# Optimization experiments

Measured on AMD Instinct MI355X. Metric: run time of the kernel, lower is better.

Reference implementation:

```python
import jax, jax.numpy as jnp
import numpy as np

DIM = 512
HEADS = 8
WIN = 64
HIDDEN = 2048
EPS = 1e-5


def layernorm(x, g, b):
    mu = jnp.mean(x, axis=-1, keepdims=True)
    var = jnp.var(x, axis=-1, keepdims=True)
    return (x - mu) * jax.lax.rsqrt(var + EPS) * g + b


def setup_inputs() -> dict:
    key = jax.random.key(0)
    ks = jax.random.split(key, 10)
    s = lambda fan_in: 1.0 / np.sqrt(fan_in)
    return {
        "x": jax.random.normal(ks[0], (8, 4096, DIM), dtype=jnp.float32),
        "ln1_g": jnp.ones((DIM,), jnp.float32),
        "ln1_b": jnp.zeros((DIM,), jnp.float32),
        "qkv_w": jax.random.normal(ks[1], (DIM, 3 * DIM), jnp.float32) * s(DIM),
        "qkv_b": jnp.zeros((3 * DIM,), jnp.float32),
        "proj_w": jax.random.normal(ks[2], (DIM, DIM), jnp.float32) * s(DIM),
        "proj_b": jnp.zeros((DIM,), jnp.float32),
        "ln2_g": jnp.ones((DIM,), jnp.float32),
        "ln2_b": jnp.zeros((DIM,), jnp.float32),
        "fc1_w": jax.random.normal(ks[3], (DIM, HIDDEN), jnp.float32) * s(DIM),
        "fc1_b": jnp.zeros((HIDDEN,), jnp.float32),
        "fc2_w": jax.random.normal(ks[4], (HIDDEN, DIM), jnp.float32) * s(HIDDEN),
        "fc2_b": jnp.zeros((DIM,), jnp.float32),
    }


def reference(x, ln1_g, ln1_b, qkv_w, qkv_b, proj_w, proj_b, ln2_g, ln2_b,
              fc1_w, fc1_b, fc2_w, fc2_b):
    B, N, C = x.shape
    hd = C // HEADS
    scale = hd ** -0.5

    # --- W-MSA (shift_size forced to 0, attn_mask None) ---
    h = layernorm(x, ln1_g, ln1_b)
    hw = h.reshape(B * (N // WIN), WIN, C)
    qkv = hw @ qkv_w + qkv_b
    qkv = qkv.reshape(-1, WIN, 3, HEADS, hd)
    q = qkv[:, :, 0] * scale
    k = qkv[:, :, 1]
    v = qkv[:, :, 2]
    attn = jnp.einsum('bqhd,bkhd->bhqk', q, k)
    attn = jax.nn.softmax(attn, axis=-1)
    o = jnp.einsum('bhqk,bkhd->bqhd', attn, v).reshape(-1, WIN, C)
    o = o @ proj_w + proj_b
    x = x + o.reshape(B, N, C)

    # --- MLP (GELU exact, dropout=0) ---
    h2 = layernorm(x, ln2_g, ln2_b)
    h2 = jax.nn.gelu(h2 @ fc1_w + fc1_b, approximate=False)
    x = x + (h2 @ fc2_w + fc2_b)
    return x
```

## Files before the change

### kernel.cpp

```cpp
#include <hip/hip_runtime.h>
#include <hip/hip_bf16.h>
#include <cstdint>

typedef unsigned short U16;
typedef float f32x4 __attribute__((ext_vector_type(4)));
typedef __bf16 bf16x8 __attribute__((ext_vector_type(8)));

#define DEVINL __device__ __forceinline__

DEVINL U16 f2bf(float f) {
    unsigned u = __float_as_uint(f);
    return (U16)((u + 0x7FFFu + ((u >> 16) & 1u)) >> 16);
}
DEVINL float bf2f(U16 s) { return __uint_as_float(((unsigned)s) << 16); }

DEVINL void gld16(const void* g, void* l) {
    __builtin_amdgcn_global_load_lds(
        (const __attribute__((address_space(1))) void*)g,
        (__attribute__((address_space(3))) void*)l, 16, 0, 0);
}

#define MFMA_BF16 __builtin_amdgcn_mfma_f32_16x16x32_bf16

__global__ __launch_bounds__(256) void tcast_kernel(const float* __restrict__ w,
                                                    U16* __restrict__ wt, int K, int N) {
    __shared__ float tile[32][33];
    int n0 = blockIdx.x * 32, k0 = blockIdx.y * 32;
    int tx = threadIdx.x, ty = threadIdx.y;
#pragma unroll
    for (int i = 0; i < 32; i += 8) tile[ty + i][tx] = w[(size_t)(k0 + ty + i) * N + (n0 + tx)];
    __syncthreads();
#pragma unroll
    for (int i = 0; i < 32; i += 8) wt[(size_t)(n0 + ty + i) * K + (k0 + tx)] = f2bf(tile[tx][ty + i]);
}

__global__ __launch_bounds__(256) void ln_kernel(const float* __restrict__ x,
                                                 const float* __restrict__ g,
                                                 const float* __restrict__ b,
                                                 U16* __restrict__ out) {
    int lane = threadIdx.x & 63;
    size_t row = (size_t)blockIdx.x * 4 + (threadIdx.x >> 6);
    const float4* xr = (const float4*)(x + row * 512);
    float4 v0 = xr[lane], v1 = xr[lane + 64];
    float s = (v0.x + v0.y) + (v0.z + v0.w) + (v1.x + v1.y) + (v1.z + v1.w);
    float sq = (v0.x * v0.x + v0.y * v0.y + v0.z * v0.z + v0.w * v0.w) +
               (v1.x * v1.x + v1.y * v1.y + v1.z * v1.z + v1.w * v1.w);
#pragma unroll
    for (int m = 1; m < 64; m <<= 1) { s += __shfl_xor(s, m); sq += __shfl_xor(sq, m); }
    float mu = s * (1.f / 512.f);
    float var = sq * (1.f / 512.f) - mu * mu;
    float rs = rsqrtf(var + 1e-5f);
    const float4* g4 = (const float4*)g;
    const float4* b4 = (const float4*)b;
    float4 gv = g4[lane], bv = b4[lane];
    ushort4 o;
    o.x = f2bf((v0.x - mu) * rs * gv.x + bv.x);
    o.y = f2bf((v0.y - mu) * rs * gv.y + bv.y);
    o.z = f2bf((v0.z - mu) * rs * gv.z + bv.z);
    o.w = f2bf((v0.w - mu) * rs * gv.w + bv.w);
    ((ushort4*)(out + row * 512))[lane] = o;
    gv = g4[lane + 64]; bv = b4[lane + 64];
    o.x = f2bf((v1.x - mu) * rs * gv.x + bv.x);
    o.y = f2bf((v1.y - mu) * rs * gv.y + bv.y);
    o.z = f2bf((v1.z - mu) * rs * gv.z + bv.z);
    o.w = f2bf((v1.w - mu) * rs * gv.w + bv.w);
    ((ushort4*)(out + row * 512))[lane + 64] = o;
}

template <int EPI>
__global__ __launch_bounds__(512, 1) void gemm256(const U16* __restrict__ A,
                                                  const U16* __restrict__ Bt,
                                                  const float* __restrict__ bias,
                                                  const float* __restrict__ resid,
                                                  U16* __restrict__ outb,
                                                  float* __restrict__ outf,
                                                  int M, int N, int K, int gridN) {
    __shared__ __align__(16) U16 smem[65536];

    const int tid = threadIdx.x;
    const int lane = tid & 63, wv = tid >> 6;
    const int lo = lane & 15, hi = lane >> 4;
    const int wm = wv >> 2, wn = wv & 3;

    const int nwg = gridDim.x, bid = blockIdx.x;
    const int swz = (bid & 7) * (nwg >> 3) + (bid >> 3);
    const int bn = swz % gridN, bm = swz / gridN;

    const int sr = tid >> 3;
    const int clog = (tid & 7) ^ (sr & 7);
    const U16* gA = A + (size_t)(bm * 256 + sr) * K + clog * 8;
    const U16* gB = Bt + (size_t)(bn * 256 + sr) * K + clog * 8;

#define STAGE_PANEL(g, off, p)                                        \
    do {                                                              \
        U16* _l = smem + (off) + (p) * 8192 + tid * 8;                \
        gld16((g) + (size_t)((p) * 128) * K, _l);                     \
        gld16((g) + (size_t)((p) * 128 + 64) * K, _l + 4096);         \
    } while (0)

    const int ck0 = ((hi) ^ (lo & 7)) << 3;
    const int ck1 = ((4 | hi) ^ (lo & 7)) << 3;

    f32x4 acc[8][4] = {};

    STAGE_PANEL(gA, 0, 0);
    STAGE_PANEL(gB, 16384, 0);
    STAGE_PANEL(gA, 0, 1);
    STAGE_PANEL(gB, 16384, 1);
    gA += 64; gB += 64;

    const int nt = K >> 6;
    for (int t = 0; t < nt; ++t) {
        const int cb = (t & 1) << 15;
        const int nb = cb ^ 32768;
        const bool pf = (t < nt - 1);

        if (pf) {
            STAGE_PANEL(gA, nb, 0);
            asm volatile("s_waitcnt vmcnt(2)" ::: "memory");
        } else {
            asm volatile("s_waitcnt vmcnt(0)" ::: "memory");
        }
        asm volatile("s_barrier" ::: "memory");

        const U16* Ab = smem + cb + (wm * 128 + lo) * 64;
        const U16* Bb = smem + cb + 16384 + (wn * 64 + lo) * 64;

        bf16x8 af[4][2], bg[4][2];
#pragma unroll
        for (int i = 0; i < 4; ++i) {
            af[i][0] = *(const bf16x8*)(Ab + i * 1024 + ck0);
            af[i][1] = *(const bf16x8*)(Ab + i * 1024 + ck1);
        }
#pragma unroll
        for (int j = 0; j < 2; ++j) {
            bg[j][0] = *(const bf16x8*)(Bb + j * 1024 + ck0);
            bg[j][1] = *(const bf16x8*)(Bb + j * 1024 + ck1);
        }
        __builtin_amdgcn_s_setprio(1);
#pragma unroll
        for (int i = 0; i < 4; ++i)
#pragma unroll
            for (int j = 0; j < 2; ++j) {
                acc[i][j] = MFMA_BF16(af[i][0], bg[j][0], acc[i][j], 0, 0, 0);
                acc[i][j] = MFMA_BF16(af[i][1], bg[j][1], acc[i][j], 0, 0, 0);
            }
        __builtin_amdgcn_s_setprio(0);

        if (pf) STAGE_PANEL(gB, nb + 16384, 0);
#pragma unroll
        for (int j = 2; j < 4; ++j) {
            bg[j][0] = *(const bf16x8*)(Bb + j * 1024 + ck0);
            bg[j][1] = *(const bf16x8*)(Bb + j * 1024 + ck1);
        }
        __builtin_amdgcn_s_setprio(1);
#pragma unroll
        for (int i = 0; i < 4; ++i)
#pragma unroll
            for (int j = 2; j < 4; ++j) {
                acc[i][j] = MFMA_BF16(af[i][0], bg[j][0], acc[i][j], 0, 0, 0);
                acc[i][j] = MFMA_BF16(af[i][1], bg[j][1], acc[i][j], 0, 0, 0);
            }
        __builtin_amdgcn_s_setprio(0);

        if (pf) STAGE_PANEL(gA, nb, 1);
#pragma unroll
        for (int i = 0; i < 4; ++i) {
            af[i][0] = *(const bf16x8*)(Ab + (i + 4) * 1024 + ck0);
            af[i][1] = *(const bf16x8*)(Ab + (i + 4) * 1024 + ck1);
        }
        __builtin_amdgcn_s_setprio(1);
#pragma unroll
        for (int i = 0; i < 4; ++i)
#pragma unroll
            for (int j = 0; j < 2; ++j) {
                acc[4 + i][j] = MFMA_BF16(af[i][0], bg[j][0], acc[4 + i][j], 0, 0, 0);
                acc[4 + i][j] = MFMA_BF16(af[i][1], bg[j][1], acc[4 + i][j], 0, 0, 0);
            }
        __builtin_amdgcn_s_setprio(0);

        if (pf) STAGE_PANEL(gB, nb + 16384, 1);
        __builtin_amdgcn_s_setprio(1);
#pragma unroll
        for (int i = 0; i < 4; ++i)
#pragma unroll
            for (int j = 2; j < 4; ++j) {
                acc[4 + i][j] = MFMA_BF16(af[i][0], bg[j][0], acc[4 + i][j], 0, 0, 0);
                acc[4 + i][j] = MFMA_BF16(af[i][1], bg[j][1], acc[4 + i][j], 0, 0, 0);
            }
        __builtin_amdgcn_s_setprio(0);

        asm volatile("s_barrier" ::: "memory");
        gA += 64; gB += 64;
    }

    const int row0 = bm * 256 + wm * 128 + hi * 4;
    const int col0 = bn * 256 + wn * 64 + lo;
    float bc[4];
#pragma unroll
    for (int j = 0; j < 4; ++j) bc[j] = bias[col0 + j * 16];

    if (EPI == 1) {
#pragma unroll
        for (int i = 0; i < 8; ++i)
#pragma unroll
            for (int r = 0; r < 4; ++r) {
                const size_t rowb = (size_t)(row0 + i * 16 + r) * N;
#pragma unroll
                for (int j = 0; j < 4; ++j) {
                    const size_t idx = rowb + col0 + j * 16;
                    outf[idx] = acc[i][j][r] + bc[j] + resid[idx];
                }
            }
    } else {
#pragma unroll
        for (int i = 0; i < 8; ++i)
#pragma unroll
            for (int j = 0; j < 4; ++j)
#pragma unroll
                for (int r = 0; r < 4; ++r) {
                    float v = acc[i][j][r] + bc[j];
                    if (EPI == 2) v = 0.5f * v * (1.f + erff(v * 0.70710678118654752f));
                    outb[(size_t)(row0 + i * 16 + r) * N + col0 + j * 16] = f2bf(v);
                }
    }
#undef STAGE_PANEL
}

__global__ __launch_bounds__(256) void attn_kernel(const U16* __restrict__ qkv,
                                                   U16* __restrict__ o) {
    const int blk = blockIdx.x;
    const int w = blk >> 3, h = blk & 7;
    const int tid = threadIdx.x;
    const int lane = tid & 63, wv = tid >> 6;
    const int lo = lane & 15, hi = lane >> 4;

    __shared__ __align__(16) U16 Qs[64][72];
    __shared__ __align__(16) U16 Ks[64][72];
    __shared__ __align__(16) U16 Vt[64][72];
    __shared__ __align__(16) U16 Ps[4][16][72];

    {
        const int r = tid >> 2;
        const int c0 = (tid & 3) << 4;
        const U16* p = qkv + (size_t)(w * 64 + r) * 1536 + h * 64 + c0;
        *(bf16x8*)&Ks[r][c0] = *(const bf16x8*)(p + 512);
        *(bf16x8*)&Ks[r][c0 + 8] = *(const bf16x8*)(p + 520);
        const U16* pv = p + 1024;
#pragma unroll
        for (int i = 0; i < 16; i++) Vt[c0 + i][r] = pv[i];
#pragma unroll
        for (int i = 0; i < 16; i++) Qs[r][c0 + i] = f2bf(bf2f(p[i]) * 0.125f);
    }
    __syncthreads();

    const int rb = wv * 16;
    f32x4 s[4] = {};
#pragma unroll
    for (int dc = 0; dc < 64; dc += 32) {
        bf16x8 a = *(const bf16x8*)&Qs[rb + lo][dc + hi * 8];
#pragma unroll
        for (int jb = 0; jb < 4; jb++) {
            bf16x8 bfr = *(const bf16x8*)&Ks[jb * 16 + lo][dc + hi * 8];
            s[jb] = MFMA_BF16(a, bfr, s[jb], 0, 0, 0);
        }
    }
#pragma unroll
    for (int r = 0; r < 4; r++) {
        float m = fmaxf(fmaxf(s[0][r], s[1][r]), fmaxf(s[2][r], s[3][r]));
#pragma unroll
        for (int msk = 1; msk < 16; msk <<= 1) m = fmaxf(m, __shfl_xor(m, msk));
        float e[4], sum = 0.f;
#pragma unroll
        for (int jb = 0; jb < 4; jb++) { e[jb] = expf(s[jb][r] - m); sum += e[jb]; }
#pragma unroll
        for (int msk = 1; msk < 16; msk <<= 1) sum += __shfl_xor(sum, msk);
        float inv = 1.f / sum;
#pragma unroll
        for (int jb = 0; jb < 4; jb++) Ps[wv][hi * 4 + r][jb * 16 + lo] = f2bf(e[jb] * inv);
    }
    __syncthreads();

    f32x4 oa[4] = {};
#pragma unroll
    for (int jc = 0; jc < 64; jc += 32) {
        bf16x8 a = *(const bf16x8*)&Ps[wv][lo][jc + hi * 8];
#pragma unroll
        for (int db = 0; db < 4; db++) {
            bf16x8 bfr = *(const bf16x8*)&Vt[db * 16 + lo][jc + hi * 8];
            oa[db] = MFMA_BF16(a, bfr, oa[db], 0, 0, 0);
        }
    }
#pragma unroll
    for (int db = 0; db < 4; db++)
#pragma unroll
        for (int r = 0; r < 4; r++)
            o[(size_t)(w * 64 + rb + hi * 4 + r) * 512 + h * 64 + db * 16 + lo] = f2bf(oa[db][r]);
}

extern "C" void kernel_launch(void* const* d_in, const int* in_sizes, int n_in,
                              void* d_out, int out_size, void* d_ws, size_t ws_size,
                              hipStream_t stream) {
    const float* x = (const float*)d_in[0];
    const float* ln1_g = (const float*)d_in[1];
    const float* ln1_b = (const float*)d_in[2];
    const float* qkv_w = (const float*)d_in[3];
    const float* qkv_b = (const float*)d_in[4];
    const float* proj_w = (const float*)d_in[5];
    const float* proj_b = (const float*)d_in[6];
    const float* ln2_g = (const float*)d_in[7];
    const float* ln2_b = (const float*)d_in[8];
    const float* fc1_w = (const float*)d_in[9];
    const float* fc1_b = (const float*)d_in[10];
    const float* fc2_w = (const float*)d_in[11];
    const float* fc2_b = (const float*)d_in[12];
    float* out = (float*)d_out;

    char* ws = (char*)d_ws;
    U16* hbuf = (U16*)ws;
    U16* big = (U16*)(ws + 33554432);
    U16* wt_qkv = (U16*)(ws + 33554432 + 134217728);
    U16* wt_proj = wt_qkv + 1536 * 512;
    U16* wt_fc1 = wt_proj + 512 * 512;
    U16* wt_fc2 = wt_fc1 + 2048 * 512;

    dim3 tb(32, 8);
    tcast_kernel<<<dim3(1536 / 32, 512 / 32), tb, 0, stream>>>(qkv_w, wt_qkv, 512, 1536);
    tcast_kernel<<<dim3(512 / 32, 512 / 32), tb, 0, stream>>>(proj_w, wt_proj, 512, 512);
    tcast_kernel<<<dim3(2048 / 32, 512 / 32), tb, 0, stream>>>(fc1_w, wt_fc1, 512, 2048);
    tcast_kernel<<<dim3(512 / 32, 2048 / 32), tb, 0, stream>>>(fc2_w, wt_fc2, 2048, 512);

    ln_kernel<<<8192, 256, 0, stream>>>(x, ln1_g, ln1_b, hbuf);
    gemm256<0><<<768, 512, 0, stream>>>(hbuf, wt_qkv, qkv_b, nullptr, big, nullptr, 32768, 1536, 512, 6);
    attn_kernel<<<4096, 256, 0, stream>>>(big, hbuf);
    gemm256<1><<<256, 512, 0, stream>>>(hbuf, wt_proj, proj_b, x, nullptr, out, 32768, 512, 512, 2);
    ln_kernel<<<8192, 256, 0, stream>>>(out, ln2_g, ln2_b, hbuf);
    gemm256<2><<<1024, 512, 0, stream>>>(hbuf, wt_fc1, fc1_b, nullptr, big, nullptr, 32768, 2048, 512, 8);
    gemm256<1><<<256, 512, 0, stream>>>(big, wt_fc2, fc2_b, out, nullptr, out, 32768, 512, 2048, 2);
}
```

Baseline: 400.5 us.

## Restructure GEMM mainloop into 4-stage ring with 32-wide K steps

The bf16 GEMM main loop now uses 32-wide K tiles in a four-buffer LDS ring and prefetches two stages ahead. This gives one barrier per iteration and one load-then-MFMA block, replacing the interleaved double-buffered 64-wide scheme. The LDS swizzle and fragment addressing are reworked to match the 32-element rows. The launch bound now asks for two blocks per CU, which caps registers per thread. Since the kernel still declares 128KB of shared memory, a second resident block is unlikely, so the tighter cap risks spills with little occupancy gain.

```diff
diff --git a/kernel.cpp b/kernel.cpp
--- a/kernel.cpp
+++ b/kernel.cpp
@@ -68,7 +68,7 @@
 }
 
 template <int EPI>
-__global__ __launch_bounds__(512, 1) void gemm256(const U16* __restrict__ A,
+__global__ __launch_bounds__(512, 2) void gemm256(const U16* __restrict__ A,
                                                   const U16* __restrict__ Bt,
                                                   const float* __restrict__ bias,
                                                   const float* __restrict__ resid,
@@ -86,112 +86,63 @@
     const int swz = (bid & 7) * (nwg >> 3) + (bid >> 3);
     const int bn = swz % gridN, bm = swz / gridN;
 
-    const int sr = tid >> 3;
-    const int clog = (tid & 7) ^ (sr & 7);
-    const U16* gA = A + (size_t)(bm * 256 + sr) * K + clog * 8;
-    const U16* gB = Bt + (size_t)(bn * 256 + sr) * K + clog * 8;
-
-#define STAGE_PANEL(g, off, p)                                        \
+    const int sr = tid >> 2;
+    const int lc = (tid & 3) ^ (sr & 3);
+    const U16* gA0 = A + (size_t)(bm * 256 + sr) * K + lc * 8;
+    const U16* gB0 = Bt + (size_t)(bn * 256 + sr) * K + lc * 8;
+
+#define STAGE(t2)                                                     \
     do {                                                              \
-        U16* _l = smem + (off) + (p) * 8192 + tid * 8;                \
-        gld16((g) + (size_t)((p) * 128) * K, _l);                     \
-        gld16((g) + (size_t)((p) * 128 + 64) * K, _l + 4096);         \
+        const int _b = ((t2) & 3) * 16384;                            \
+        const U16* _ga = gA0 + (size_t)(t2) * 32;                     \
+        const U16* _gb = gB0 + (size_t)(t2) * 32;                     \
+        U16* _la = smem + _b + tid * 8;                               \
+        U16* _lb = smem + _b + 8192 + tid * 8;                        \
+        gld16(_ga, _la);                                              \
+        gld16(_ga + (size_t)128 * K, _la + 4096);                     \
+        gld16(_gb, _lb);                                              \
+        gld16(_gb + (size_t)128 * K, _lb + 4096);                     \
     } while (0)
 
-    const int ck0 = ((hi) ^ (lo & 7)) << 3;
-    const int ck1 = ((4 | hi) ^ (lo & 7)) << 3;
+    const int ck = (hi ^ (lo & 3)) << 3;
 
     f32x4 acc[8][4] = {};
 
-    STAGE_PANEL(gA, 0, 0);
-    STAGE_PANEL(gB, 16384, 0);
-    STAGE_PANEL(gA, 0, 1);
-    STAGE_PANEL(gB, 16384, 1);
-    gA += 64; gB += 64;
-
-    const int nt = K >> 6;
+    const int nt = K >> 5;
+    STAGE(0);
+    STAGE(1);
+
     for (int t = 0; t < nt; ++t) {
-        const int cb = (t & 1) << 15;
-        const int nb = cb ^ 32768;
-        const bool pf = (t < nt - 1);
-
-        if (pf) {
-            STAGE_PANEL(gA, nb, 0);
-            asm volatile("s_waitcnt vmcnt(2)" ::: "memory");
+        if (t + 2 < nt) {
+            STAGE(t + 2);
+            asm volatile("s_waitcnt vmcnt(8)" ::: "memory");
+        } else if (t + 1 < nt) {
+            asm volatile("s_waitcnt vmcnt(4)" ::: "memory");
         } else {
             asm volatile("s_waitcnt vmcnt(0)" ::: "memory");
         }
         asm volatile("s_barrier" ::: "memory");
 
-        const U16* Ab = smem + cb + (wm * 128 + lo) * 64;
-        const U16* Bb = smem + cb + 16384 + (wn * 64 + lo) * 64;
-
-        bf16x8 af[4][2], bg[4][2];
-#pragma unroll
-        for (int i = 0; i < 4; ++i) {
-            af[i][0] = *(const bf16x8*)(Ab + i * 1024 + ck0);
-            af[i][1] = *(const bf16x8*)(Ab + i * 1024 + ck1);
-        }
-#pragma unroll
-        for (int j = 0; j < 2; ++j) {
-            bg[j][0] = *(const bf16x8*)(Bb + j * 1024 + ck0);
-            bg[j][1] = *(const bf16x8*)(Bb + j * 1024 + ck1);
-        }
+        const int cb = (t & 3) * 16384;
+        const U16* Abuf = smem + cb + wm * 4096;
+        const U16* Bbuf = smem + cb + 8192 + (wn >> 1) * 4096;
+        const int brow = (wn & 1) * 64;
+
+        bf16x8 af[8], bg[4];
+#pragma unroll
+        for (int j = 0; j < 4; ++j)
+            bg[j] = *(const bf16x8*)(Bbuf + (brow + j * 16 + lo) * 32 + ck);
+#pragma unroll
+        for (int i = 0; i < 8; ++i)
+            af[i] = *(const bf16x8*)(Abuf + (i * 16 + lo) * 32 + ck);
+
         __builtin_amdgcn_s_setprio(1);
 #pragma unroll
-        for (int i = 0; i < 4; ++i)
-#pragma unroll
-            for (int j = 0; j < 2; ++j) {
-                acc[i][j] = MFMA_BF16(af[i][0], bg[j][0], acc[i][j], 0, 0, 0);
-                acc[i][j] = MFMA_BF16(af[i][1], bg[j][1], acc[i][j], 0, 0, 0);
-            }
+        for (int i = 0; i < 8; ++i)
+#pragma unroll
+            for (int j = 0; j < 4; ++j)
+                acc[i][j] = MFMA_BF16(af[i], bg[j], acc[i][j], 0, 0, 0);
         __builtin_amdgcn_s_setprio(0);
-
-        if (pf) STAGE_PANEL(gB, nb + 16384, 0);
-#pragma unroll
-        for (int j = 2; j < 4; ++j) {
-            bg[j][0] = *(const bf16x8*)(Bb + j * 1024 + ck0);
-            bg[j][1] = *(const bf16x8*)(Bb + j * 1024 + ck1);
-        }
-        __builtin_amdgcn_s_setprio(1);
-#pragma unroll
-        for (int i = 0; i < 4; ++i)
-#pragma unroll
-            for (int j = 2; j < 4; ++j) {
-                acc[i][j] = MFMA_BF16(af[i][0], bg[j][0], acc[i][j], 0, 0, 0);
-                acc[i][j] = MFMA_BF16(af[i][1], bg[j][1], acc[i][j], 0, 0, 0);
-            }
-        __builtin_amdgcn_s_setprio(0);
-
-        if (pf) STAGE_PANEL(gA, nb, 1);
-#pragma unroll
-        for (int i = 0; i < 4; ++i) {
-            af[i][0] = *(const bf16x8*)(Ab + (i + 4) * 1024 + ck0);
-            af[i][1] = *(const bf16x8*)(Ab + (i + 4) * 1024 + ck1);
-        }
-        __builtin_amdgcn_s_setprio(1);
-#pragma unroll
-        for (int i = 0; i < 4; ++i)
-#pragma unroll
-            for (int j = 0; j < 2; ++j) {
-                acc[4 + i][j] = MFMA_BF16(af[i][0], bg[j][0], acc[4 + i][j], 0, 0, 0);
-                acc[4 + i][j] = MFMA_BF16(af[i][1], bg[j][1], acc[4 + i][j], 0, 0, 0);
-            }
-        __builtin_amdgcn_s_setprio(0);
-
-        if (pf) STAGE_PANEL(gB, nb + 16384, 1);
-        __builtin_amdgcn_s_setprio(1);
-#pragma unroll
-        for (int i = 0; i < 4; ++i)
-#pragma unroll
-            for (int j = 2; j < 4; ++j) {
-                acc[4 + i][j] = MFMA_BF16(af[i][0], bg[j][0], acc[4 + i][j], 0, 0, 0);
-                acc[4 + i][j] = MFMA_BF16(af[i][1], bg[j][1], acc[4 + i][j], 0, 0, 0);
-            }
-        __builtin_amdgcn_s_setprio(0);
-
-        asm volatile("s_barrier" ::: "memory");
-        gA += 64; gB += 64;
     }
 
     const int row0 = bm * 256 + wm * 128 + hi * 4;
@@ -224,7 +175,7 @@
                     outb[(size_t)(row0 + i * 16 + r) * N + col0 + j * 16] = f2bf(v);
                 }
     }
-#undef STAGE_PANEL
+#undef STAGE
 }
 
 __global__ __launch_bounds__(256) void attn_kernel(const U16* __restrict__ qkv,
```

Result: slower. 413.5 us (+3.3%).

## Restructure GEMM prefetch schedule with per-phase barriers and full vmcnt wait

Applied to the files above, without the earlier changes.

Reorganizes the double-buffered GEMM main loop so that the next tile's A and B panels are issued as whole-matrix loads after the current LDS fragments are read, with computed per-iteration addresses instead of advancing pointers. It adds s_barrier calls between each MFMA phase and waits for all outstanding global loads at the top of each iteration. The intent is a more regular, ping-pong-style schedule that keeps waves in lockstep and overlaps loads with compute. In exchange it adds several barriers per iteration and drops the partial vmcnt overlap, which may stall on memory latency.

```diff
diff --git a/kernel.cpp b/kernel.cpp
--- a/kernel.cpp
+++ b/kernel.cpp
@@ -88,14 +88,15 @@
 
     const int sr = tid >> 3;
     const int clog = (tid & 7) ^ (sr & 7);
-    const U16* gA = A + (size_t)(bm * 256 + sr) * K + clog * 8;
-    const U16* gB = Bt + (size_t)(bn * 256 + sr) * K + clog * 8;
-
-#define STAGE_PANEL(g, off, p)                                        \
-    do {                                                              \
-        U16* _l = smem + (off) + (p) * 8192 + tid * 8;                \
-        gld16((g) + (size_t)((p) * 128) * K, _l);                     \
-        gld16((g) + (size_t)((p) * 128 + 64) * K, _l + 4096);         \
+    const U16* gA0 = A + (size_t)(bm * 256 + sr) * K + clog * 8;
+    const U16* gB0 = Bt + (size_t)(bn * 256 + sr) * K + clog * 8;
+
+#define STAGE_H(g0, matoff, h, t1)                                              \
+    do {                                                                        \
+        U16* _l = smem + (((t1) & 1) << 15) + (matoff) + (h) * 8192 + tid * 8;  \
+        const U16* _g = (g0) + (size_t)(t1) * 64 + (size_t)((h) * 128) * K;     \
+        gld16(_g, _l);                                                          \
+        gld16(_g + (size_t)64 * K, _l + 4096);                                  \
     } while (0)
 
     const int ck0 = ((hi) ^ (lo & 7)) << 3;
@@ -103,30 +104,23 @@
 
     f32x4 acc[8][4] = {};
 
-    STAGE_PANEL(gA, 0, 0);
-    STAGE_PANEL(gB, 16384, 0);
-    STAGE_PANEL(gA, 0, 1);
-    STAGE_PANEL(gB, 16384, 1);
-    gA += 64; gB += 64;
-
     const int nt = K >> 6;
+    STAGE_H(gA0, 0, 0, 0);
+    STAGE_H(gA0, 0, 1, 0);
+    STAGE_H(gB0, 16384, 0, 0);
+    STAGE_H(gB0, 16384, 1, 0);
+
     for (int t = 0; t < nt; ++t) {
         const int cb = (t & 1) << 15;
-        const int nb = cb ^ 32768;
-        const bool pf = (t < nt - 1);
-
-        if (pf) {
-            STAGE_PANEL(gA, nb, 0);
-            asm volatile("s_waitcnt vmcnt(2)" ::: "memory");
-        } else {
-            asm volatile("s_waitcnt vmcnt(0)" ::: "memory");
-        }
-        asm volatile("s_barrier" ::: "memory");
+        const bool pf = (t + 1 < nt);
+        asm volatile("s_waitcnt vmcnt(0)" ::: "memory");
+        __builtin_amdgcn_s_barrier();
 
         const U16* Ab = smem + cb + (wm * 128 + lo) * 64;
         const U16* Bb = smem + cb + 16384 + (wn * 64 + lo) * 64;
 
         bf16x8 af[4][2], bg[4][2];
+
 #pragma unroll
         for (int i = 0; i < 4; ++i) {
             af[i][0] = *(const bf16x8*)(Ab + i * 1024 + ck0);
@@ -137,6 +131,12 @@
             bg[j][0] = *(const bf16x8*)(Bb + j * 1024 + ck0);
             bg[j][1] = *(const bf16x8*)(Bb + j * 1024 + ck1);
         }
+        if (pf) {
+            STAGE_H(gA0, 0, 0, t + 1);
+            STAGE_H(gA0, 0, 1, t + 1);
+        }
+        __builtin_amdgcn_s_barrier();
+        asm volatile("s_waitcnt lgkmcnt(0)" ::: "memory");
         __builtin_amdgcn_s_setprio(1);
 #pragma unroll
         for (int i = 0; i < 4; ++i)
@@ -146,13 +146,19 @@
                 acc[i][j] = MFMA_BF16(af[i][1], bg[j][1], acc[i][j], 0, 0, 0);
             }
         __builtin_amdgcn_s_setprio(0);
-
-        if (pf) STAGE_PANEL(gB, nb + 16384, 0);
+        __builtin_amdgcn_s_barrier();
+
 #pragma unroll
         for (int j = 2; j < 4; ++j) {
             bg[j][0] = *(const bf16x8*)(Bb + j * 1024 + ck0);
             bg[j][1] = *(const bf16x8*)(Bb + j * 1024 + ck1);
         }
+        if (pf) {
+            STAGE_H(gB0, 16384, 0, t + 1);
+            STAGE_H(gB0, 16384, 1, t + 1);
+        }
+        __builtin_amdgcn_s_barrier();
+        asm volatile("s_waitcnt lgkmcnt(0)" ::: "memory");
         __builtin_amdgcn_s_setprio(1);
 #pragma unroll
         for (int i = 0; i < 4; ++i)
@@ -162,13 +168,15 @@
                 acc[i][j] = MFMA_BF16(af[i][1], bg[j][1], acc[i][j], 0, 0, 0);
             }
         __builtin_amdgcn_s_setprio(0);
-
-        if (pf) STAGE_PANEL(gA, nb, 1);
+        __builtin_amdgcn_s_barrier();
+
 #pragma unroll
         for (int i = 0; i < 4; ++i) {
             af[i][0] = *(const bf16x8*)(Ab + (i + 4) * 1024 + ck0);
             af[i][1] = *(const bf16x8*)(Ab + (i + 4) * 1024 + ck1);
         }
+        __builtin_amdgcn_s_barrier();
+        asm volatile("s_waitcnt lgkmcnt(0)" ::: "memory");
         __builtin_amdgcn_s_setprio(1);
 #pragma unroll
         for (int i = 0; i < 4; ++i)
@@ -178,8 +186,8 @@
                 acc[4 + i][j] = MFMA_BF16(af[i][1], bg[j][1], acc[4 + i][j], 0, 0, 0);
             }
         __builtin_amdgcn_s_setprio(0);
-
-        if (pf) STAGE_PANEL(gB, nb + 16384, 1);
+        __builtin_amdgcn_s_barrier();
+
         __builtin_amdgcn_s_setprio(1);
 #pragma unroll
         for (int i = 0; i < 4; ++i)
@@ -189,9 +197,6 @@
                 acc[4 + i][j] = MFMA_BF16(af[i][1], bg[j][1], acc[4 + i][j], 0, 0, 0);
             }
         __builtin_amdgcn_s_setprio(0);
-
-        asm volatile("s_barrier" ::: "memory");
-        gA += 64; gB += 64;
     }
 
     const int row0 = bm * 256 + wm * 128 + hi * 4;
@@ -224,7 +229,7 @@
                     outb[(size_t)(row0 + i * 16 + r) * N + col0 + j * 16] = f2bf(v);
                 }
     }
-#undef STAGE_PANEL
+#undef STAGE_H
 }
 
 __global__ __launch_bounds__(256) void attn_kernel(const U16* __restrict__ qkv,
```

Measured after the change: 399.1 us. No clear change (-0.3%).
